# Kernel tuning notes

Measured on AMD Instinct MI355X. Metric: run time of the kernel, lower is better.

Reference implementation:

```python
import jax, jax.numpy as jnp
import numpy as np

B = 4            # batch
L = 4096         # max_len
D_MODEL = 1024   # qkv_dim == out_features
H = 16           # num_heads
SEG = 64         # max_seg_len
HD = D_MODEL // H          # head_dim = 64
NSEG = L // SEG            # num segments = 64
NEG = -1e10


def setup_inputs() -> dict:
    key = jax.random.key(0)
    k0, k1, k2, k3, k4 = jax.random.split(key, 5)
    scale = 1.0 / np.sqrt(D_MODEL).astype(np.float32)
    x = jax.random.normal(k0, (B, L, D_MODEL), jnp.float32)
    wq = jax.random.normal(k1, (D_MODEL, H, HD), jnp.float32) * scale
    wk = jax.random.normal(k2, (D_MODEL, H, HD), jnp.float32) * scale
    wv = jax.random.normal(k3, (D_MODEL, H, HD), jnp.float32) * scale
    wo = jax.random.normal(k4, (H, HD, D_MODEL), jnp.float32) * scale
    return {"input_qkv": x, "wq": wq, "wk": wk, "wv": wv, "wo": wo}


def reference(input_qkv, wq, wk, wv, wo):
    inv_sqrt_hd = 1.0 / np.sqrt(HD).astype(np.float32)
    # QKV projections; query pre-scaled by 1/sqrt(head_dim) as in get_qkv
    q = jnp.einsum('bld,dhf->blhf', input_qkv, wq) * inv_sqrt_hd
    k = jnp.einsum('bld,dhf->blhf', input_qkv, wk)
    v = jnp.einsum('bld,dhf->blhf', input_qkv, wv)

    cq = q.reshape(B * NSEG, SEG, H, HD)
    ck = k.reshape(B * NSEG, SEG, H, HD)
    cv = v.reshape(B * NSEG, SEG, H, HD)

    # Pooled per-segment query attends over its own segment's keys/values.
    # Original: merged_query = max(cq)*sqrt(HD), then flax dot_product_attention
    # rescales by 1/sqrt(HD) -> the two scalings cancel, so use max(cq) directly.
    mq = jnp.max(cq, axis=1, keepdims=True)                    # [B*NSEG, 1, H, HD]
    s_logits = jnp.einsum('bqhd,bkhd->bhqk', mq, ck)
    s_w = jax.nn.softmax(s_logits, axis=-1)
    s = jnp.einsum('bhqk,bkhd->bqhd', s_w, cv)                  # [B*NSEG, 1, H, HD]
    span_val = s.reshape(B, NSEG, H, HD)
    span_key = jnp.max(ck, axis=1).reshape(B, NSEG, H, HD)

    # Local causal attention logits within each segment
    causal = jnp.tril(jnp.ones((SEG, SEG), bool))
    local_bias = jnp.where(causal, 0.0, NEG).astype(jnp.float32)[None, :, None, :]
    local_logits = jnp.einsum('bqhd,bkhd->bqhk', cq, ck) + local_bias
    local_logits = local_logits.reshape(B, L, H, SEG)

    # Cross-segment logits: each token attends to strictly earlier segment summaries
    seg_id = jnp.arange(NSEG)
    prev_bias = jnp.where(seg_id[:, None] > seg_id[None, :], 0.0, NEG).astype(jnp.float32)
    prev_bias = jnp.repeat(prev_bias, SEG, axis=0)[None, :, None, :]  # [1, L, 1, NSEG]
    prev_logits = jnp.einsum('bqhd,bkhd->bqhk', q, span_key) + prev_bias

    # Joint softmax over [local keys | previous-segment summaries]
    joint = jnp.concatenate([local_logits, prev_logits], axis=-1)   # [B, L, H, SEG+NSEG]
    w = jax.nn.softmax(joint, axis=-1)
    local_att = w[..., :SEG].reshape(B * NSEG, SEG, H, SEG)
    prev_att = w[..., SEG:]

    local_merged = jnp.einsum('bqhk,bkhd->bqhd', local_att, cv).reshape(B, L, H, HD)
    prev_merged = jnp.einsum('bqhk,bkhd->bqhd', prev_att, span_val)

    return jnp.einsum('blhd,hdf->blf', local_merged + prev_merged, wo)
```

## Files before the change

### kernel.cpp

```cpp
#include <hip/hip_runtime.h>

#define BB    4
#define LL    4096
#define DM    1024
#define HH    16
#define SEGC  64
#define HDC   64
#define NSEGC 64
#define NEGV  -1.0e10f

typedef __bf16 bf16x8 __attribute__((ext_vector_type(8)));
typedef float  f32x4  __attribute__((ext_vector_type(4)));

__device__ __forceinline__ float bf2f(unsigned short s) {
  union { unsigned int u; float f; } x; x.u = ((unsigned int)s) << 16; return x.f;
}
__device__ __forceinline__ unsigned short f2bf(float f) {
  union { float f; unsigned int u; } x; x.f = f;
  unsigned int u = x.u;
  return (unsigned short)((u + 0x7fffu + ((u >> 16) & 1u)) >> 16);
}

__device__ __forceinline__ void gl2lds16(const unsigned short* g, unsigned short* l) {
  __builtin_amdgcn_global_load_lds(
      (const __attribute__((address_space(1))) unsigned int*)g,
      (__attribute__((address_space(3))) unsigned int*)l,
      16, 0, 0);
}

__device__ __forceinline__ void g2lds16(unsigned short* dst, const unsigned short* src) {
  int4 a = *(const int4*)(src);
  int4 b = *(const int4*)(src + 8);
  unsigned int* d = (unsigned int*)dst;
  const unsigned int* pa = (const unsigned int*)&a;
  const unsigned int* pb = (const unsigned int*)&b;
  d[0]=pa[0]; d[1]=pa[1]; d[2]=pa[2]; d[3]=pa[3];
  d[4]=pb[0]; d[5]=pb[1]; d[6]=pb[2]; d[7]=pb[3];
}

__global__ __launch_bounds__(256) void cvt_x(const float* __restrict__ x,
                                             unsigned short* __restrict__ xb) {
  const size_t i = ((size_t)blockIdx.x * 256 + threadIdx.x) * 8;
  float4 a = *(const float4*)(x + i);
  float4 b = *(const float4*)(x + i + 4);
  unsigned short o[8];
  o[0]=f2bf(a.x); o[1]=f2bf(a.y); o[2]=f2bf(a.z); o[3]=f2bf(a.w);
  o[4]=f2bf(b.x); o[5]=f2bf(b.y); o[6]=f2bf(b.z); o[7]=f2bf(b.w);
  *(int4*)(xb + i) = *(const int4*)o;
}

__global__ __launch_bounds__(256) void transpose_w(
    const float* __restrict__ wq, const float* __restrict__ wk,
    const float* __restrict__ wv, const float* __restrict__ wo,
    unsigned short* __restrict__ WqkvT, unsigned short* __restrict__ woT) {
  __shared__ unsigned short TS[64 * 65];

  const int z  = blockIdx.z;
  const int bx = blockIdx.x;
  const int by = blockIdx.y;
  const int t  = threadIdx.x;

  const float* src; unsigned short* dst; float scale = 1.0f;
  if (z == 0)      { src = wq; dst = WqkvT;               scale = 0.125f; }
  else if (z == 1) { src = wk; dst = WqkvT + 1024 * 1024; }
  else if (z == 2) { src = wv; dst = WqkvT + 2048 * 1024; }
  else             { src = wo; dst = woT; }

  const int rr = t >> 4;
  const int c4 = (t & 15) * 4;
  #pragma unroll
  for (int it = 0; it < 4; it++) {
    const int r = it * 16 + rr;
    float4 f = *(const float4*)(src + (size_t)(by * 64 + r) * 1024 + bx * 64 + c4);
    TS[(c4 + 0) * 65 + r] = f2bf(f.x * scale);
    TS[(c4 + 1) * 65 + r] = f2bf(f.y * scale);
    TS[(c4 + 2) * 65 + r] = f2bf(f.z * scale);
    TS[(c4 + 3) * 65 + r] = f2bf(f.w * scale);
  }
  __syncthreads();

  const int wr = t >> 3;
  const int w8 = (t & 7) * 8;
  #pragma unroll
  for (int it = 0; it < 2; it++) {
    const int n = it * 32 + wr;
    unsigned short o[8];
    #pragma unroll
    for (int j = 0; j < 8; j++) o[j] = TS[n * 65 + w8 + j];
    *(int4*)(dst + (size_t)(bx * 64 + n) * 1024 + by * 64 + w8) = *(const int4*)o;
  }
}

template <bool C_F32>
__global__ __launch_bounds__(512, 2) void gemm256(
    const unsigned short* __restrict__ A,
    const unsigned short* __restrict__ Bt,
    void* __restrict__ Cv,
    int ldc)
{
  __shared__ __align__(16) unsigned short L[2][2][4][4096];

  const int t    = threadIdx.x;
  const int wave = t >> 6;
  const int lane = t & 63;
  const int l15  = lane & 15;
  const int q4   = lane >> 4;
  const int wm   = wave >> 2;
  const int wn   = wave & 3;

  const int nwg = gridDim.x;
  const int wg  = blockIdx.x;
  const int swz = (wg & 7) * (nwg >> 3) + (wg >> 3);
  const int m0  = (swz & 63) << 8;
  const int n0  = (swz >> 6) << 8;

  const int srow = ((wave >> 1) << 4) + (lane >> 2);
  const int scol = ((wave & 1) << 5) + (((lane & 3) << 3) ^ (((lane >> 5) & 1) << 4));
  const size_t laneoff = (size_t)srow * 1024 + scol;
  const unsigned short* Ab = A  + (size_t)m0 * 1024 + laneoff;
  const unsigned short* Bb = Bt + (size_t)n0 * 1024 + laneoff;

  const int rdoff = l15 * 32 + ((q4 * 8) ^ (((l15 >> 3) & 1) << 4));

#define SA_(d, q, kt) gl2lds16(Ab + ((size_t)(q) * 64) * 1024 + (size_t)(kt) * 64, \
                               &L[d][0][q][0] + wave * 512)
#define SB_(d, q, kt) gl2lds16(Bb + ((size_t)(q) * 64) * 1024 + (size_t)(kt) * 64, \
                               &L[d][1][q][0] + wave * 512)
#define LDA8(d, i, kk) (*(const bf16x8*)(&L[d][0][wm * 2 + ((i) >> 2)][0] + \
                        ((((i) & 3) * 2 + (kk)) * 512) + rdoff))
#define LDB8(d, j, kk) (*(const bf16x8*)(&L[d][1][wn][0] + \
                        ((((j) * 2 + (kk))) * 512) + rdoff))
#define BAR()   asm volatile("s_barrier" ::: "memory")
#define LGKM0() asm volatile("s_waitcnt lgkmcnt(0)" ::: "memory")
#define VMW(n)  asm volatile("s_waitcnt vmcnt(" #n ")" ::: "memory")
#define MFMA_(av, bv, cv) __builtin_amdgcn_mfma_f32_16x16x32_bf16(av, bv, cv, 0, 0, 0)

  f32x4 acc[8][4];
  #pragma unroll
  for (int i = 0; i < 8; ++i)
    #pragma unroll
    for (int j = 0; j < 4; ++j) acc[i][j] = (f32x4){0.f, 0.f, 0.f, 0.f};

  SB_(0,0,0); SB_(0,1,0); SB_(0,2,0); SB_(0,3,0); SA_(0,0,0); SA_(0,2,0);
  SA_(0,1,0); SA_(0,3,0);
  SB_(1,0,1); SB_(1,1,1); SB_(1,2,1); SB_(1,3,1); SA_(1,0,1); SA_(1,2,1);
  VMW(8); BAR();

  #pragma unroll 1
  for (int it = 0; it < 8; ++it) {
    const int t1 = 2 * it + 1;
    const int s2 = (2 * it + 2) & 15;
    const int s3 = (2 * it + 3) & 15;
    bf16x8 a[4][2], b[4][2];

    #pragma unroll
    for (int ii = 0; ii < 4; ++ii) { a[ii][0] = LDA8(0, ii, 0); a[ii][1] = LDA8(0, ii, 1); }
    #pragma unroll
    for (int jj = 0; jj < 4; ++jj) { b[jj][0] = LDB8(0, jj, 0); b[jj][1] = LDB8(0, jj, 1); }
    SA_(1, 1, t1); SA_(1, 3, t1);
    BAR(); LGKM0();
    __builtin_amdgcn_s_setprio(1);
    #pragma unroll
    for (int ii = 0; ii < 4; ++ii)
      #pragma unroll
      for (int jj = 0; jj < 2; ++jj) {
        acc[ii][jj] = MFMA_(a[ii][0], b[jj][0], acc[ii][jj]);
        acc[ii][jj] = MFMA_(a[ii][1], b[jj][1], acc[ii][jj]);
      }
    __builtin_amdgcn_s_setprio(0);
    BAR();

    SB_(0, 0, s2); SB_(0, 1, s2);
    BAR();
    __builtin_amdgcn_s_setprio(1);
    #pragma unroll
    for (int ii = 0; ii < 4; ++ii)
      #pragma unroll
      for (int jj = 2; jj < 4; ++jj) {
        acc[ii][jj] = MFMA_(a[ii][0], b[jj][0], acc[ii][jj]);
        acc[ii][jj] = MFMA_(a[ii][1], b[jj][1], acc[ii][jj]);
      }
    __builtin_amdgcn_s_setprio(0);
    VMW(10); BAR();

    #pragma unroll
    for (int ii = 0; ii < 4; ++ii) { a[ii][0] = LDA8(0, 4 + ii, 0); a[ii][1] = LDA8(0, 4 + ii, 1); }
    SB_(0, 2, s2); SB_(0, 3, s2);
    BAR(); LGKM0();
    __builtin_amdgcn_s_setprio(1);
    #pragma unroll
    for (int ii = 0; ii < 4; ++ii)
      #pragma unroll
      for (int jj = 2; jj < 4; ++jj) {
        acc[4 + ii][jj] = MFMA_(a[ii][0], b[jj][0], acc[4 + ii][jj]);
        acc[4 + ii][jj] = MFMA_(a[ii][1], b[jj][1], acc[4 + ii][jj]);
      }
    __builtin_amdgcn_s_setprio(0);
    BAR();

    SA_(0, 0, s2); SA_(0, 2, s2);
    BAR();
    __builtin_amdgcn_s_setprio(1);
    #pragma unroll
    for (int ii = 0; ii < 4; ++ii)
      #pragma unroll
      for (int jj = 0; jj < 2; ++jj) {
        acc[4 + ii][jj] = MFMA_(a[ii][0], b[jj][0], acc[4 + ii][jj]);
        acc[4 + ii][jj] = MFMA_(a[ii][1], b[jj][1], acc[4 + ii][jj]);
      }
    __builtin_amdgcn_s_setprio(0);
    VMW(8); BAR();

    #pragma unroll
    for (int ii = 0; ii < 4; ++ii) { a[ii][0] = LDA8(1, ii, 0); a[ii][1] = LDA8(1, ii, 1); }
    #pragma unroll
    for (int jj = 0; jj < 4; ++jj) { b[jj][0] = LDB8(1, jj, 0); b[jj][1] = LDB8(1, jj, 1); }
    SA_(0, 1, s2); SA_(0, 3, s2);
    BAR(); LGKM0();
    __builtin_amdgcn_s_setprio(1);
    #pragma unroll
    for (int ii = 0; ii < 4; ++ii)
      #pragma unroll
      for (int jj = 0; jj < 2; ++jj) {
        acc[ii][jj] = MFMA_(a[ii][0], b[jj][0], acc[ii][jj]);
        acc[ii][jj] = MFMA_(a[ii][1], b[jj][1], acc[ii][jj]);
      }
    __builtin_amdgcn_s_setprio(0);
    BAR();

    SB_(1, 0, s3); SB_(1, 1, s3);
    BAR();
    __builtin_amdgcn_s_setprio(1);
    #pragma unroll
    for (int ii = 0; ii < 4; ++ii)
      #pragma unroll
      for (int jj = 2; jj < 4; ++jj) {
        acc[ii][jj] = MFMA_(a[ii][0], b[jj][0], acc[ii][jj]);
        acc[ii][jj] = MFMA_(a[ii][1], b[jj][1], acc[ii][jj]);
      }
    __builtin_amdgcn_s_setprio(0);
    VMW(10); BAR();

    #pragma unroll
    for (int ii = 0; ii < 4; ++ii) { a[ii][0] = LDA8(1, 4 + ii, 0); a[ii][1] = LDA8(1, 4 + ii, 1); }
    SB_(1, 2, s3); SB_(1, 3, s3);
    BAR(); LGKM0();
    __builtin_amdgcn_s_setprio(1);
    #pragma unroll
    for (int ii = 0; ii < 4; ++ii)
      #pragma unroll
      for (int jj = 2; jj < 4; ++jj) {
        acc[4 + ii][jj] = MFMA_(a[ii][0], b[jj][0], acc[4 + ii][jj]);
        acc[4 + ii][jj] = MFMA_(a[ii][1], b[jj][1], acc[4 + ii][jj]);
      }
    __builtin_amdgcn_s_setprio(0);
    BAR();

    SA_(1, 0, s3); SA_(1, 2, s3);
    BAR();
    __builtin_amdgcn_s_setprio(1);
    #pragma unroll
    for (int ii = 0; ii < 4; ++ii)
      #pragma unroll
      for (int jj = 0; jj < 2; ++jj) {
        acc[4 + ii][jj] = MFMA_(a[ii][0], b[jj][0], acc[4 + ii][jj]);
        acc[4 + ii][jj] = MFMA_(a[ii][1], b[jj][1], acc[4 + ii][jj]);
      }
    __builtin_amdgcn_s_setprio(0);
    VMW(8); BAR();
  }

  #pragma unroll
  for (int i = 0; i < 8; ++i) {
    #pragma unroll
    for (int j = 0; j < 4; ++j) {
      const int col = n0 + wn * 64 + j * 16 + l15;
      #pragma unroll
      for (int r = 0; r < 4; ++r) {
        const int row = m0 + wm * 128 + i * 16 + q4 * 4 + r;
        if (C_F32) ((float*)Cv)[(size_t)row * ldc + col] = acc[i][j][r];
        else ((unsigned short*)Cv)[(size_t)row * ldc + col] = f2bf(acc[i][j][r]);
      }
    }
  }
  VMW(0);

#undef SA_
#undef SB_
#undef LDA8
#undef LDB8
#undef BAR
#undef LGKM0
#undef VMW
#undef MFMA_
}

__global__ __launch_bounds__(64) void span_kernel(
    const unsigned short* __restrict__ qkv,
    unsigned short* __restrict__ spanK,
    unsigned short* __restrict__ spanV)
{
  __shared__ unsigned short QS[64 * 66], KS[64 * 66], VS[64 * 66];
  __shared__ float mqs[64], ws[64];

  const int c = blockIdx.x;
  const int h = blockIdx.y;
  const int b = c >> 6, n = c & 63;
  const int t = threadIdx.x;

  const size_t rowbase = ((size_t)(b * LL + n * SEGC + t)) * 3072 + h * 64;
  #pragma unroll
  for (int j = 0; j < 4; j++) {
    g2lds16(QS + t * 66 + j * 16, qkv + rowbase + j * 16);
    g2lds16(KS + t * 66 + j * 16, qkv + rowbase + 1024 + j * 16);
    g2lds16(VS + t * 66 + j * 16, qkv + rowbase + 2048 + j * 16);
  }
  __syncthreads();

  float mq = -3.0e38f, sk = -3.0e38f;
  for (int r = 0; r < 64; r++) {
    mq = fmaxf(mq, bf2f(QS[r * 66 + t]));
    sk = fmaxf(sk, bf2f(KS[r * 66 + t]));
  }
  mqs[t] = mq;
  spanK[((size_t)c * 16 + h) * 64 + t] = f2bf(sk);
  __syncthreads();

  float logit = 0.f;
  for (int d = 0; d < 64; d++) logit += mqs[d] * bf2f(KS[t * 66 + d]);
  float m = logit;
  #pragma unroll
  for (int off = 32; off; off >>= 1) m = fmaxf(m, __shfl_xor(m, off, 64));
  float e = __expf(logit - m);
  float s = e;
  #pragma unroll
  for (int off = 32; off; off >>= 1) s += __shfl_xor(s, off, 64);
  ws[t] = e / s;
  __syncthreads();

  float sv = 0.f;
  for (int kk = 0; kk < 64; kk++) sv += ws[kk] * bf2f(VS[kk * 66 + t]);
  spanV[((size_t)c * 16 + h) * 64 + t] = f2bf(sv);
}

__global__ __launch_bounds__(256) void attn_kernel(
    const unsigned short* __restrict__ qkv,
    const unsigned short* __restrict__ spanK,
    const unsigned short* __restrict__ spanV,
    unsigned short* __restrict__ att)
{
  __shared__ unsigned short VT[64 * 136];
  __shared__ unsigned short WL[64 * 136];

  const int c = blockIdx.x;
  const int h = blockIdx.y;
  const int b = c >> 6, n = c & 63;
  const int t = threadIdx.x;
  const int wave = t >> 6;
  const int lane = t & 63;
  const int l15  = lane & 15;
  const int q4   = lane >> 4;

  #pragma unroll
  for (int it = 0; it < 4; it++) {
    const int idx = t + 256 * it;
    const int kp  = idx >> 3;
    const int fc  = (idx & 7) * 8;
    const unsigned short* src;
    if (kp < 64)
      src = qkv + ((size_t)(b * LL + n * SEGC + kp)) * 3072 + 2048 + h * 64 + fc;
    else
      src = spanV + ((size_t)(b * 64 + (kp - 64)) * 16 + h) * 64 + fc;
    int4 val = *(const int4*)src;
    const unsigned short* e = (const unsigned short*)&val;
    #pragma unroll
    for (int i = 0; i < 8; i++) VT[(fc + i) * 136 + kp] = e[i];
  }

  bf16x8 af[2];
  {
    const size_t qbase = ((size_t)(b * LL + n * SEGC + wave * 16 + l15)) * 3072
                         + h * 64 + q4 * 8;
    af[0] = *(const bf16x8*)(qkv + qbase);
    af[1] = *(const bf16x8*)(qkv + qbase + 32);
  }

  f32x4 accl[8];
  #pragma unroll
  for (int tt = 0; tt < 8; tt++) accl[tt] = (f32x4){0.f, 0.f, 0.f, 0.f};

  #pragma unroll
  for (int s = 0; s < 2; s++) {
    bf16x8 bfr[8];
    #pragma unroll
    for (int tt = 0; tt < 8; tt++) {
      const unsigned short* src;
      if (tt < 4)
        src = qkv + ((size_t)(b * LL + n * SEGC + tt * 16 + l15)) * 3072
              + 1024 + h * 64 + s * 32 + q4 * 8;
      else
        src = spanK + ((size_t)((b * 64 + (tt - 4) * 16 + l15) * 16 + h)) * 64
              + s * 32 + q4 * 8;
      bfr[tt] = *(const bf16x8*)src;
    }
    #pragma unroll
    for (int tt = 0; tt < 8; tt++)
      accl[tt] = __builtin_amdgcn_mfma_f32_16x16x32_bf16(af[s], bfr[tt], accl[tt], 0, 0, 0);
  }

  #pragma unroll
  for (int tt = 0; tt < 8; tt++) {
    const int col = (tt & 3) * 16 + l15;
    #pragma unroll
    for (int rr = 0; rr < 4; rr++) {
      const int r_att = wave * 16 + q4 * 4 + rr;
      const bool valid = (tt < 4) ? (col <= r_att) : (col < n);
      if (!valid) accl[tt][rr] = NEGV;
    }
  }

  #pragma unroll
  for (int rr = 0; rr < 4; rr++) {
    float mx = accl[0][rr];
    #pragma unroll
    for (int tt = 1; tt < 8; tt++) mx = fmaxf(mx, accl[tt][rr]);
    #pragma unroll
    for (int msk = 1; msk < 16; msk <<= 1) mx = fmaxf(mx, __shfl_xor(mx, msk, 64));
    float sm = 0.f;
    float ex[8];
    #pragma unroll
    for (int tt = 0; tt < 8; tt++) { ex[tt] = __expf(accl[tt][rr] - mx); sm += ex[tt]; }
    #pragma unroll
    for (int msk = 1; msk < 16; msk <<= 1) sm += __shfl_xor(sm, msk, 64);
    const float inv = 1.0f / sm;
    const int r_att = wave * 16 + q4 * 4 + rr;
    #pragma unroll
    for (int tt = 0; tt < 8; tt++) {
      const int colj = (tt < 4) ? (tt * 16 + l15) : (64 + (tt - 4) * 16 + l15);
      WL[r_att * 136 + colj] = f2bf(ex[tt] * inv);
    }
  }

  __syncthreads();

  f32x4 accm[4];
  #pragma unroll
  for (int j = 0; j < 4; j++) accm[j] = (f32x4){0.f, 0.f, 0.f, 0.f};
  #pragma unroll
  for (int s = 0; s < 4; s++) {
    const bf16x8 aw = *(const bf16x8*)(WL + (wave * 16 + l15) * 136 + s * 32 + q4 * 8);
    #pragma unroll
    for (int j = 0; j < 4; j++) {
      const bf16x8 bv = *(const bf16x8*)(VT + (j * 16 + l15) * 136 + s * 32 + q4 * 8);
      accm[j] = __builtin_amdgcn_mfma_f32_16x16x32_bf16(aw, bv, accm[j], 0, 0, 0);
    }
  }

  #pragma unroll
  for (int j = 0; j < 4; j++) {
    #pragma unroll
    for (int rr = 0; rr < 4; rr++) {
      const int row = wave * 16 + q4 * 4 + rr;
      const int col = j * 16 + l15;
      att[((size_t)(b * LL + n * SEGC + row)) * 1024 + h * 64 + col] = f2bf(accm[j][rr]);
    }
  }
}

extern "C" void kernel_launch(void* const* d_in, const int* in_sizes, int n_in,
                              void* d_out, int out_size, void* d_ws, size_t ws_size,
                              hipStream_t stream) {
  const float* x  = (const float*)d_in[0];
  const float* wq = (const float*)d_in[1];
  const float* wk = (const float*)d_in[2];
  const float* wv = (const float*)d_in[3];
  const float* wo = (const float*)d_in[4];
  float* out = (float*)d_out;

  unsigned short* wsp   = (unsigned short*)d_ws;
  unsigned short* xb    = wsp;
  unsigned short* qkv   = xb + 16777216;
  unsigned short* WqkvT = qkv + 50331648;
  unsigned short* woT   = WqkvT + 3145728;
  unsigned short* skb   = woT + 1048576;
  unsigned short* svb   = skb + 262144;
  unsigned short* attb  = xb;

  cvt_x<<<8192, 256, 0, stream>>>(x, xb);
  transpose_w<<<dim3(16, 16, 4), 256, 0, stream>>>(wq, wk, wv, wo, WqkvT, woT);
  gemm256<false><<<768, 512, 0, stream>>>(xb, WqkvT, (void*)qkv, 3072);
  span_kernel<<<dim3(256, 16), 64, 0, stream>>>(qkv, skb, svb);
  attn_kernel<<<dim3(256, 16), 256, 0, stream>>>(qkv, skb, svb, attb);
  gemm256<true><<<256, 512, 0, stream>>>(attb, woT, (void*)out, 1024);
}
```

Before: 344.0 us.

## Reorder GEMM prefetch schedule, split summary reductions, swizzle VT in LDS

The GEMM main loop now issues A-tile global-to-LDS loads before B tiles. It splits the B-fragment LDS reads across two phases and adjusts the vmcnt waits, so loads overlap better with MFMA work. The segment-summary kernel splits its max, dot and weighted-sum reductions into two independent accumulators with unrolling to shorten dependency chains. The attention kernel XOR-swizzles the transposed V layout in shared memory to reduce bank conflicts on the scattered writes and the MFMA operand reads. The reordered waits risk races if the vmcnt counts do not match the new issue order.

```diff
diff --git a/kernel.cpp b/kernel.cpp
--- a/kernel.cpp
+++ b/kernel.cpp
@@ -141,22 +141,22 @@
     #pragma unroll
     for (int j = 0; j < 4; ++j) acc[i][j] = (f32x4){0.f, 0.f, 0.f, 0.f};
 
-  SB_(0,0,0); SB_(0,1,0); SB_(0,2,0); SB_(0,3,0); SA_(0,0,0); SA_(0,2,0);
+  SA_(0,0,0); SA_(0,2,0); SB_(0,0,0); SB_(0,1,0); SB_(0,2,0); SB_(0,3,0);
   SA_(0,1,0); SA_(0,3,0);
-  SB_(1,0,1); SB_(1,1,1); SB_(1,2,1); SB_(1,3,1); SA_(1,0,1); SA_(1,2,1);
-  VMW(8); BAR();
+  SA_(1,0,1); SA_(1,2,1); SB_(1,0,1); SB_(1,1,1); SB_(1,2,1); SB_(1,3,1);
+  VMW(6); BAR();
 
   #pragma unroll 1
   for (int it = 0; it < 8; ++it) {
     const int t1 = 2 * it + 1;
-    const int s2 = (2 * it + 2) & 15;
-    const int s3 = (2 * it + 3) & 15;
+    const int t2 = (2 * it + 2) & 15;
+    const int t3 = (2 * it + 3) & 15;
     bf16x8 a[4][2], b[4][2];
 
     #pragma unroll
     for (int ii = 0; ii < 4; ++ii) { a[ii][0] = LDA8(0, ii, 0); a[ii][1] = LDA8(0, ii, 1); }
     #pragma unroll
-    for (int jj = 0; jj < 4; ++jj) { b[jj][0] = LDB8(0, jj, 0); b[jj][1] = LDB8(0, jj, 1); }
+    for (int jj = 0; jj < 2; ++jj) { b[jj][0] = LDB8(0, jj, 0); b[jj][1] = LDB8(0, jj, 1); }
     SA_(1, 1, t1); SA_(1, 3, t1);
     BAR(); LGKM0();
     __builtin_amdgcn_s_setprio(1);
@@ -170,8 +170,10 @@
     __builtin_amdgcn_s_setprio(0);
     BAR();
 
-    SB_(0, 0, s2); SB_(0, 1, s2);
-    BAR();
+    #pragma unroll
+    for (int jj = 2; jj < 4; ++jj) { b[jj][0] = LDB8(0, jj, 0); b[jj][1] = LDB8(0, jj, 1); }
+    SA_(0, 0, t2); SA_(0, 2, t2);
+    BAR(); LGKM0();
     __builtin_amdgcn_s_setprio(1);
     #pragma unroll
     for (int ii = 0; ii < 4; ++ii)
@@ -181,11 +183,11 @@
         acc[ii][jj] = MFMA_(a[ii][1], b[jj][1], acc[ii][jj]);
       }
     __builtin_amdgcn_s_setprio(0);
-    VMW(10); BAR();
+    BAR();
 
     #pragma unroll
     for (int ii = 0; ii < 4; ++ii) { a[ii][0] = LDA8(0, 4 + ii, 0); a[ii][1] = LDA8(0, 4 + ii, 1); }
-    SB_(0, 2, s2); SB_(0, 3, s2);
+    SB_(0, 0, t2); SB_(0, 1, t2);
     BAR(); LGKM0();
     __builtin_amdgcn_s_setprio(1);
     #pragma unroll
@@ -198,7 +200,7 @@
     __builtin_amdgcn_s_setprio(0);
     BAR();
 
-    SA_(0, 0, s2); SA_(0, 2, s2);
+    SB_(0, 2, t2); SB_(0, 3, t2);
     BAR();
     __builtin_amdgcn_s_setprio(1);
     #pragma unroll
@@ -209,13 +211,13 @@
         acc[4 + ii][jj] = MFMA_(a[ii][1], b[jj][1], acc[4 + ii][jj]);
       }
     __builtin_amdgcn_s_setprio(0);
-    VMW(8); BAR();
+    VMW(6); BAR();
 
     #pragma unroll
     for (int ii = 0; ii < 4; ++ii) { a[ii][0] = LDA8(1, ii, 0); a[ii][1] = LDA8(1, ii, 1); }
     #pragma unroll
-    for (int jj = 0; jj < 4; ++jj) { b[jj][0] = LDB8(1, jj, 0); b[jj][1] = LDB8(1, jj, 1); }
-    SA_(0, 1, s2); SA_(0, 3, s2);
+    for (int jj = 0; jj < 2; ++jj) { b[jj][0] = LDB8(1, jj, 0); b[jj][1] = LDB8(1, jj, 1); }
+    SA_(0, 1, t2); SA_(0, 3, t2);
     BAR(); LGKM0();
     __builtin_amdgcn_s_setprio(1);
     #pragma unroll
@@ -228,8 +230,10 @@
     __builtin_amdgcn_s_setprio(0);
     BAR();
 
-    SB_(1, 0, s3); SB_(1, 1, s3);
-    BAR();
+    #pragma unroll
+    for (int jj = 2; jj < 4; ++jj) { b[jj][0] = LDB8(1, jj, 0); b[jj][1] = LDB8(1, jj, 1); }
+    SA_(1, 0, t3); SA_(1, 2, t3);
+    BAR(); LGKM0();
     __builtin_amdgcn_s_setprio(1);
     #pragma unroll
     for (int ii = 0; ii < 4; ++ii)
@@ -239,11 +243,11 @@
         acc[ii][jj] = MFMA_(a[ii][1], b[jj][1], acc[ii][jj]);
       }
     __builtin_amdgcn_s_setprio(0);
-    VMW(10); BAR();
+    BAR();
 
     #pragma unroll
     for (int ii = 0; ii < 4; ++ii) { a[ii][0] = LDA8(1, 4 + ii, 0); a[ii][1] = LDA8(1, 4 + ii, 1); }
-    SB_(1, 2, s3); SB_(1, 3, s3);
+    SB_(1, 0, t3); SB_(1, 1, t3);
     BAR(); LGKM0();
     __builtin_amdgcn_s_setprio(1);
     #pragma unroll
@@ -256,7 +260,7 @@
     __builtin_amdgcn_s_setprio(0);
     BAR();
 
-    SA_(1, 0, s3); SA_(1, 2, s3);
+    SB_(1, 2, t3); SB_(1, 3, t3);
     BAR();
     __builtin_amdgcn_s_setprio(1);
     #pragma unroll
@@ -267,7 +271,7 @@
         acc[4 + ii][jj] = MFMA_(a[ii][1], b[jj][1], acc[4 + ii][jj]);
       }
     __builtin_amdgcn_s_setprio(0);
-    VMW(8); BAR();
+    VMW(6); BAR();
   }
 
   #pragma unroll
@@ -317,17 +321,25 @@
   }
   __syncthreads();
 
-  float mq = -3.0e38f, sk = -3.0e38f;
-  for (int r = 0; r < 64; r++) {
-    mq = fmaxf(mq, bf2f(QS[r * 66 + t]));
-    sk = fmaxf(sk, bf2f(KS[r * 66 + t]));
-  }
-  mqs[t] = mq;
-  spanK[((size_t)c * 16 + h) * 64 + t] = f2bf(sk);
+  float mqa = -3.0e38f, mqb = -3.0e38f, ska = -3.0e38f, skc = -3.0e38f;
+  #pragma unroll 8
+  for (int r = 0; r < 64; r += 2) {
+    mqa = fmaxf(mqa, bf2f(QS[r * 66 + t]));
+    mqb = fmaxf(mqb, bf2f(QS[(r + 1) * 66 + t]));
+    ska = fmaxf(ska, bf2f(KS[r * 66 + t]));
+    skc = fmaxf(skc, bf2f(KS[(r + 1) * 66 + t]));
+  }
+  mqs[t] = fmaxf(mqa, mqb);
+  spanK[((size_t)c * 16 + h) * 64 + t] = f2bf(fmaxf(ska, skc));
   __syncthreads();
 
-  float logit = 0.f;
-  for (int d = 0; d < 64; d++) logit += mqs[d] * bf2f(KS[t * 66 + d]);
+  float l0 = 0.f, l1 = 0.f;
+  #pragma unroll 8
+  for (int d = 0; d < 64; d += 2) {
+    l0 += mqs[d] * bf2f(KS[t * 66 + d]);
+    l1 += mqs[d + 1] * bf2f(KS[t * 66 + d + 1]);
+  }
+  float logit = l0 + l1;
   float m = logit;
   #pragma unroll
   for (int off = 32; off; off >>= 1) m = fmaxf(m, __shfl_xor(m, off, 64));
@@ -338,9 +350,13 @@
   ws[t] = e / s;
   __syncthreads();
 
-  float sv = 0.f;
-  for (int kk = 0; kk < 64; kk++) sv += ws[kk] * bf2f(VS[kk * 66 + t]);
-  spanV[((size_t)c * 16 + h) * 64 + t] = f2bf(sv);
+  float sv0 = 0.f, sv1 = 0.f;
+  #pragma unroll 8
+  for (int kk = 0; kk < 64; kk += 2) {
+    sv0 += ws[kk] * bf2f(VS[kk * 66 + t]);
+    sv1 += ws[kk + 1] * bf2f(VS[(kk + 1) * 66 + t]);
+  }
+  spanV[((size_t)c * 16 + h) * 64 + t] = f2bf(sv0 + sv1);
 }
 
 __global__ __launch_bounds__(256) void attn_kernel(
@@ -373,8 +389,13 @@
       src = spanV + ((size_t)(b * 64 + (kp - 64)) * 16 + h) * 64 + fc;
     int4 val = *(const int4*)src;
     const unsigned short* e = (const unsigned short*)&val;
-    #pragma unroll
-    for (int i = 0; i < 8; i++) VT[(fc + i) * 136 + kp] = e[i];
+    const int kb = kp >> 3;
+    #pragma unroll
+    for (int i = 0; i < 8; i++) {
+      const int f  = fc + i;
+      const int nb = (kb & 8) | ((kb ^ (f >> 3)) & 7);
+      VT[f * 136 + nb * 8 + (kp & 7)] = e[i];
+    }
   }
 
   bf16x8 af[2];
@@ -451,7 +472,10 @@
     const bf16x8 aw = *(const bf16x8*)(WL + (wave * 16 + l15) * 136 + s * 32 + q4 * 8);
     #pragma unroll
     for (int j = 0; j < 4; j++) {
-      const bf16x8 bv = *(const bf16x8*)(VT + (j * 16 + l15) * 136 + s * 32 + q4 * 8);
+      const int f  = j * 16 + l15;
+      const int kb = s * 4 + q4;
+      const int nb = (kb & 8) | ((kb ^ (f >> 3)) & 7);
+      const bf16x8 bv = *(const bf16x8*)(VT + f * 136 + nb * 8);
       accm[j] = __builtin_amdgcn_mfma_f32_16x16x32_bf16(aw, bv, accm[j], 0, 0, 0);
     }
   }
```

After: 346.3 us. Within noise of the previous version (+0.7%).
